# Optimization experiments

Hardware: AMD Instinct MI355X
Metric: run time of the kernel (lower is better)

Reference implementation:

```python
import jax, jax.numpy as jnp
from jax import lax
import numpy as np

NPOINT = 1024
RADIUS = 0.25
NSAMPLE = 32
USE_XYZ = True


def setup_inputs() -> dict:
    key = jax.random.key(0)
    k1, k2 = jax.random.split(key)
    xyz = jax.random.normal(k1, (8, 8192, 3), dtype=jnp.float32)
    points = jax.random.normal(k2, (8, 8192, 32), dtype=jnp.float32)
    return {"xyz": xyz, "points": points}


def furthest_point_sample(xyz, npoint):
    """Iterative FPS; returns (B, npoint, 3) sampled coordinates.
    Matches torch reference: seeded with xyz[:, 0], squared-distance metric."""
    B, N, _ = xyz.shape
    first = xyz[:, 0]  # (B, 3)
    d0 = jnp.full((B, N), 1e38, dtype=xyz.dtype)

    def step(carry, _):
        dist, last = carry  # dist: (B,N), last: (B,3)
        d2 = jnp.sum((xyz - last[:, None, :]) ** 2, axis=-1)  # (B,N)
        dist = jnp.minimum(dist, d2)
        idx = jnp.argmax(dist, axis=1)  # (B,)
        nxt = jnp.take_along_axis(xyz, idx[:, None, None], axis=1)[:, 0]  # (B,3)
        return (dist, nxt), nxt

    _, outs = lax.scan(step, (d0, first), None, length=npoint - 1)  # (npoint-1, B, 3)
    return jnp.concatenate([first[None], outs], axis=0).transpose(1, 0, 2)  # (B,npoint,3)


def ball_query(radius, nsample, xyz, new_xyz):
    """First `nsample` indices within `radius` of each center (ascending index
    order), padded with the first found index — matches pointnet2 CUDA kernel.
    Returns (B, npoint, nsample) int32."""
    N = xyz.shape[1]
    d2 = jnp.sum((new_xyz[:, :, None, :] - xyz[:, None, :, :]) ** 2, axis=-1)  # (B,npoint,N)
    mask = d2 < radius * radius
    ar = jnp.arange(N, dtype=jnp.int32)
    # top_k on negated indices -> smallest valid indices first
    score = jnp.where(mask, -ar, jnp.int32(-(N + 1)))
    vals, _ = lax.top_k(score, nsample)  # (B,npoint,nsample), descending
    valid = vals > -(N + 1)
    idx = jnp.where(valid, -vals, -vals[..., :1])  # pad with first hit
    return idx.astype(jnp.int32)


def group_points(points, idx):
    """points (B,N,C), idx (B,npoint,nsample) -> (B,npoint,nsample,C)."""
    B, npoint, nsample = idx.shape
    C = points.shape[-1]
    flat = idx.reshape(B, npoint * nsample)  # (B, npoint*nsample)
    g = jnp.take_along_axis(points, flat[:, :, None], axis=1)
    return g.reshape(B, npoint, nsample, C)


def reference(xyz, points):
    new_xyz = furthest_point_sample(xyz, NPOINT)  # (B,npoint,3)
    idx = ball_query(RADIUS, NSAMPLE, xyz, new_xyz)  # (B,npoint,nsample)
    grouped_xyz = group_points(xyz, idx) - new_xyz[:, :, None, :]  # center-relative
    grouped_points = group_points(points, idx)
    if USE_XYZ:
        new_points = jnp.concatenate([grouped_xyz, grouped_points], axis=-1)
    else:
        new_points = grouped_points
    return new_xyz, new_points
```

## Files before the change

kernel.cpp:

```cpp
#include <hip/hip_runtime.h>

#define BATCH   8
#define NPTS    8192
#define NPOINT  1024
#define NSAMPLE 32
#define CHANC   32
#define OUTC    35
#define R2      0.0625f

typedef float v2f __attribute__((ext_vector_type(2)));

template <int CTRL>
__device__ __forceinline__ float dpp_max_step(float v) {
    int r = __builtin_amdgcn_update_dpp(__float_as_int(v), __float_as_int(v),
                                        CTRL, 0xf, 0xf, false);
    return fmaxf(v, __int_as_float(r));
}
#define DPP_ROW_SHR(n)  (0x110 | (n))
#define DPP_BCAST15     0x142
#define DPP_BCAST31     0x143

__device__ __forceinline__ unsigned long long u64max(unsigned long long a,
                                                     unsigned long long b) {
    return a > b ? a : b;
}

__global__ __launch_bounds__(512) void fps_kernel(const float* __restrict__ xyz,
                                                  float* __restrict__ new_xyz) {
#pragma clang fp contract(off)
    const int b    = blockIdx.x;
    const int t    = threadIdx.x;
    const int lane = t & 63;
    const int w    = t >> 6;
    const float* bx = xyz + (size_t)b * NPTS * 3;

    __shared__ float4 pts[NPTS];
    __shared__ unsigned long long partial[2][8];

    v2f px[8], py[8], pz[8], dist[8];
    {
        float f[48];
        float4* fq = (float4*)f;
        const float4* s4 = (const float4*)bx + t * 12;
#pragma unroll
        for (int q = 0; q < 12; ++q) fq[q] = s4[q];
#pragma unroll
        for (int p = 0; p < 8; ++p) {
            px[p] = (v2f){f[6 * p + 0], f[6 * p + 3]};
            py[p] = (v2f){f[6 * p + 1], f[6 * p + 4]};
            pz[p] = (v2f){f[6 * p + 2], f[6 * p + 5]};
            dist[p] = (v2f){1e38f, 1e38f};
        }
#pragma unroll
        for (int i = 0; i < 16; ++i) {
            const int j  = t * 16 + i;
            const int js = j ^ ((j >> 4) & 7);
            pts[js] = make_float4(f[3 * i + 0], f[3 * i + 1], f[3 * i + 2], 0.0f);
        }
    }
    __syncthreads();

    float4 c0 = pts[0];
    float lx = c0.x, ly = c0.y, lz = c0.z;
    if (t == 0) {
        float* o = new_xyz + (size_t)b * NPOINT * 3;
        o[0] = lx; o[1] = ly; o[2] = lz;
    }

    for (int s = 1; s < NPOINT; ++s) {
        const v2f lx2 = (v2f){lx, lx};
        const v2f ly2 = (v2f){ly, ly};
        const v2f lz2 = (v2f){lz, lz};
        float bestv = -1.0f;
        int   bi    = 0;
#pragma unroll
        for (int p = 0; p < 8; ++p) {
            const v2f dx = px[p] - lx2;
            const v2f dy = py[p] - ly2;
            const v2f dz = pz[p] - lz2;
            const v2f d2 = (dx * dx + dy * dy) + dz * dz;
            const float d0 = fminf(dist[p].x, d2.x);
            const float d1 = fminf(dist[p].y, d2.y);
            dist[p] = (v2f){d0, d1};
            if (d0 > bestv) { bestv = d0; bi = 2 * p; }
            if (d1 > bestv) { bestv = d1; bi = 2 * p + 1; }
        }
        const int besti = (t << 4) + bi;

        float v = bestv;
        v = dpp_max_step<DPP_ROW_SHR(1)>(v);
        v = dpp_max_step<DPP_ROW_SHR(2)>(v);
        v = dpp_max_step<DPP_ROW_SHR(4)>(v);
        v = dpp_max_step<DPP_ROW_SHR(8)>(v);
        v = dpp_max_step<DPP_BCAST15>(v);
        v = dpp_max_step<DPP_BCAST31>(v);
        const float smax = __int_as_float(__builtin_amdgcn_readlane(__float_as_int(v), 63));

        const unsigned long long m = __ballot(bestv == smax);
        const int par = s & 1;
        if (lane == (int)__builtin_ctzll(m)) {
            partial[par][w] = ((unsigned long long)__float_as_uint(smax) << 32)
                              | (unsigned)(~besti);
        }
        __syncthreads();

        const unsigned long long* P = partial[par];
        const unsigned long long a0 = P[0], a1 = P[1], a2 = P[2], a3 = P[3];
        const unsigned long long a4 = P[4], a5 = P[5], a6 = P[6], a7 = P[7];
        const unsigned long long bp =
            u64max(u64max(u64max(a0, a1), u64max(a2, a3)),
                   u64max(u64max(a4, a5), u64max(a6, a7)));
        const int idx = (int)(~(unsigned)bp);
        const int js  = idx ^ ((idx >> 4) & 7);
        const float4 cw = pts[js];
        lx = cw.x; ly = cw.y; lz = cw.z;
        if (t == 0) {
            float* o = new_xyz + ((size_t)b * NPOINT + s) * 3;
            o[0] = lx; o[1] = ly; o[2] = lz;
        }
    }
}

__global__ __launch_bounds__(256) void ballgroup_kernel(const float* __restrict__ xyz,
                                                        const float* __restrict__ points,
                                                        const float* __restrict__ new_xyz,
                                                        float* __restrict__ out) {
#pragma clang fp contract(off)
    const int lane = threadIdx.x & 63;
    const int w    = threadIdx.x >> 6;
    const int gw   = blockIdx.x * 4 + w;
    const int b    = gw >> 10;

    const float* bx  = xyz + (size_t)b * NPTS * 3;
    const float* cen = new_xyz + (size_t)gw * 3;
    const float cx = cen[0], cy = cen[1], cz = cen[2];

    __shared__ int idxbuf[4][NSAMPLE];

    int k = 0;
    for (int base = 0; base < NPTS; base += 128) {
        const int j0 = base + lane;
        const int j1 = j0 + 64;
        const float a0 = bx[j0 * 3 + 0], a1 = bx[j0 * 3 + 1], a2 = bx[j0 * 3 + 2];
        const float c0 = bx[j1 * 3 + 0], c1 = bx[j1 * 3 + 1], c2 = bx[j1 * 3 + 2];
        const float dxa = a0 - cx, dya = a1 - cy, dza = a2 - cz;
        const float d2a = (dxa * dxa + dya * dya) + dza * dza;
        const float dxb = c0 - cx, dyb = c1 - cy, dzb = c2 - cz;
        const float d2b = (dxb * dxb + dyb * dyb) + dzb * dzb;
        const bool inA = d2a < R2;
        const bool inB = d2b < R2;

        const unsigned long long mA = __ballot(inA);
        int pre = __popcll(mA & ((1ull << lane) - 1ull));
        if (inA && (k + pre) < NSAMPLE) idxbuf[w][k + pre] = j0;
        k += __popcll(mA);
        if (k >= NSAMPLE) { k = NSAMPLE; break; }

        const unsigned long long mB = __ballot(inB);
        pre = __popcll(mB & ((1ull << lane) - 1ull));
        if (inB && (k + pre) < NSAMPLE) idxbuf[w][k + pre] = j1;
        k += __popcll(mB);
        if (k >= NSAMPLE) { k = NSAMPLE; break; }
    }
    const int first = idxbuf[w][0];

    float*       o    = out + (size_t)gw * NSAMPLE * OUTC;
    const float* prow = points + (size_t)b * NPTS * CHANC;
    for (int e = lane; e < NSAMPLE * OUTC; e += 64) {
        const int s = e / OUTC;
        const int c = e - s * OUTC;
        const int j = (s < k) ? idxbuf[w][s] : first;
        float v;
        if (c < 3) {
            const float cc = (c == 0) ? cx : (c == 1) ? cy : cz;
            v = bx[j * 3 + c] - cc;
        } else {
            v = prow[j * CHANC + (c - 3)];
        }
        o[e] = v;
    }
}

extern "C" void kernel_launch(void* const* d_in, const int* in_sizes, int n_in,
                              void* d_out, int out_size, void* d_ws, size_t ws_size,
                              hipStream_t stream) {
    const float* xyz    = (const float*)d_in[0];
    const float* points = (const float*)d_in[1];
    float* new_xyz    = (float*)d_out;
    float* new_points = new_xyz + (size_t)BATCH * NPOINT * 3;

    fps_kernel<<<BATCH, 512, 0, stream>>>(xyz, new_xyz);
    ballgroup_kernel<<<(BATCH * NPOINT) / 4, 256, 0, stream>>>(xyz, points, new_xyz, new_points);
}
```

Measured before the change: 1.006 ms.

## Split ball-query scan across four waves per center and merge results

Each block now handles one query center instead of four. Its four waves each scan a quarter of the 8192 points, keeping up to 32 in-radius hits per quarter, and the ordered concatenation of those lists gives the first 32 indices. The gather/output loop is then spread across all 256 threads. The aim is to shorten the serial scan per center, which stops early only after 32 hits and otherwise reads all points, at the cost of four times as many blocks, a block barrier, and waves scanning their quarters even when an earlier quarter already holds 32 hits.

```diff
diff --git a/kernel.cpp b/kernel.cpp
--- a/kernel.cpp
+++ b/kernel.cpp
@@ -126,19 +126,22 @@
                                                         const float* __restrict__ new_xyz,
                                                         float* __restrict__ out) {
 #pragma clang fp contract(off)
-    const int lane = threadIdx.x & 63;
-    const int w    = threadIdx.x >> 6;
-    const int gw   = blockIdx.x * 4 + w;
+    const int tid  = threadIdx.x;
+    const int lane = tid & 63;
+    const int r    = tid >> 6;
+    const int gw   = blockIdx.x;
     const int b    = gw >> 10;
 
     const float* bx  = xyz + (size_t)b * NPTS * 3;
     const float* cen = new_xyz + (size_t)gw * 3;
     const float cx = cen[0], cy = cen[1], cz = cen[2];
 
-    __shared__ int idxbuf[4][NSAMPLE];
+    __shared__ int qidx[4][NSAMPLE];
+    __shared__ int qcnt[4];
 
     int k = 0;
-    for (int base = 0; base < NPTS; base += 128) {
+    const int qbase = r << 11;
+    for (int base = qbase; base < qbase + 2048; base += 128) {
         const int j0 = base + lane;
         const int j1 = j0 + 64;
         const float a0 = bx[j0 * 3 + 0], a1 = bx[j0 * 3 + 1], a2 = bx[j0 * 3 + 2];
@@ -150,26 +153,43 @@
         const bool inA = d2a < R2;
         const bool inB = d2b < R2;
 
-        const unsigned long long mA = __ballot(inA);
-        int pre = __popcll(mA & ((1ull << lane) - 1ull));
-        if (inA && (k + pre) < NSAMPLE) idxbuf[w][k + pre] = j0;
-        k += __popcll(mA);
-        if (k >= NSAMPLE) { k = NSAMPLE; break; }
-
-        const unsigned long long mB = __ballot(inB);
-        pre = __popcll(mB & ((1ull << lane) - 1ull));
-        if (inB && (k + pre) < NSAMPLE) idxbuf[w][k + pre] = j1;
-        k += __popcll(mB);
-        if (k >= NSAMPLE) { k = NSAMPLE; break; }
-    }
-    const int first = idxbuf[w][0];
+        if (__any(inA || inB)) {
+            const unsigned long long mA = __ballot(inA);
+            int pre = __popcll(mA & ((1ull << lane) - 1ull));
+            if (inA && (k + pre) < NSAMPLE) qidx[r][k + pre] = j0;
+            k += __popcll(mA);
+            if (k >= NSAMPLE) { k = NSAMPLE; break; }
+
+            const unsigned long long mB = __ballot(inB);
+            pre = __popcll(mB & ((1ull << lane) - 1ull));
+            if (inB && (k + pre) < NSAMPLE) qidx[r][k + pre] = j1;
+            k += __popcll(mB);
+            if (k >= NSAMPLE) { k = NSAMPLE; break; }
+        }
+    }
+    if (lane == 0) qcnt[r] = k;
+    __syncthreads();
+
+    const int c0n = qcnt[0], c1n = qcnt[1], c2n = qcnt[2], c3n = qcnt[3];
+    const int o1 = c0n, o2 = c0n + c1n, o3 = o2 + c2n;
+    const int total = o3 + c3n;
+    const int kk = total < NSAMPLE ? total : NSAMPLE;
+    const int r0 = (c0n > 0) ? 0 : (c1n > 0) ? 1 : (c2n > 0) ? 2 : 3;
+    const int firstIdx = qidx[r0][0];
 
     float*       o    = out + (size_t)gw * NSAMPLE * OUTC;
     const float* prow = points + (size_t)b * NPTS * CHANC;
-    for (int e = lane; e < NSAMPLE * OUTC; e += 64) {
+    for (int e = tid; e < NSAMPLE * OUTC; e += 256) {
         const int s = e / OUTC;
         const int c = e - s * OUTC;
-        const int j = (s < k) ? idxbuf[w][s] : first;
+        int j;
+        if (s < kk) {
+            const int rr  = (int)(s >= o1) + (int)(s >= o2) + (int)(s >= o3);
+            const int off = (rr == 0) ? 0 : (rr == 1) ? o1 : (rr == 2) ? o2 : o3;
+            j = qidx[rr][s - off];
+        } else {
+            j = firstIdx;
+        }
         float v;
         if (c < 3) {
             const float cc = (c == 0) ? cx : (c == 1) ? cy : cz;
@@ -190,5 +210,5 @@
     float* new_points = new_xyz + (size_t)BATCH * NPOINT * 3;
 
     fps_kernel<<<BATCH, 512, 0, stream>>>(xyz, new_xyz);
-    ballgroup_kernel<<<(BATCH * NPOINT) / 4, 256, 0, stream>>>(xyz, points, new_xyz, new_points);
-}
+    ballgroup_kernel<<<BATCH * NPOINT, 256, 0, stream>>>(xyz, points, new_xyz, new_points);
+}
```

Result: no change. 1.005 ms (-0.0%).

## Stage point chunks in LDS and share them across many ball-query centers

Applied to the files above, without the earlier changes.

The ball-query kernel now handles 32 centers per block, 8 per wave. It stages 2048-point chunks of xyz into shared memory as float4 so that every point load is reused across many centers. Before, each wave scanned global xyz alone for a single center. The cost is far fewer blocks (one per 32 centers), which lowers occupancy. The scan also loses its early exit: the loop keeps visiting every chunk even after all 8 centers have filled their 32 samples, and only the per-center work is skipped.

```diff
diff --git a/kernel.cpp b/kernel.cpp
--- a/kernel.cpp
+++ b/kernel.cpp
@@ -7,6 +7,8 @@
 #define CHANC   32
 #define OUTC    35
 #define R2      0.0625f
+#define GCTR    32
+#define CHUNK   2048
 
 typedef float v2f __attribute__((ext_vector_type(2)));
 
@@ -126,58 +128,77 @@
                                                         const float* __restrict__ new_xyz,
                                                         float* __restrict__ out) {
 #pragma clang fp contract(off)
-    const int lane = threadIdx.x & 63;
-    const int w    = threadIdx.x >> 6;
-    const int gw   = blockIdx.x * 4 + w;
-    const int b    = gw >> 10;
-
-    const float* bx  = xyz + (size_t)b * NPTS * 3;
-    const float* cen = new_xyz + (size_t)gw * 3;
-    const float cx = cen[0], cy = cen[1], cz = cen[2];
-
-    __shared__ int idxbuf[4][NSAMPLE];
-
-    int k = 0;
-    for (int base = 0; base < NPTS; base += 128) {
-        const int j0 = base + lane;
-        const int j1 = j0 + 64;
-        const float a0 = bx[j0 * 3 + 0], a1 = bx[j0 * 3 + 1], a2 = bx[j0 * 3 + 2];
-        const float c0 = bx[j1 * 3 + 0], c1 = bx[j1 * 3 + 1], c2 = bx[j1 * 3 + 2];
-        const float dxa = a0 - cx, dya = a1 - cy, dza = a2 - cz;
-        const float d2a = (dxa * dxa + dya * dya) + dza * dza;
-        const float dxb = c0 - cx, dyb = c1 - cy, dzb = c2 - cz;
-        const float d2b = (dxb * dxb + dyb * dyb) + dzb * dzb;
-        const bool inA = d2a < R2;
-        const bool inB = d2b < R2;
-
-        const unsigned long long mA = __ballot(inA);
-        int pre = __popcll(mA & ((1ull << lane) - 1ull));
-        if (inA && (k + pre) < NSAMPLE) idxbuf[w][k + pre] = j0;
-        k += __popcll(mA);
-        if (k >= NSAMPLE) { k = NSAMPLE; break; }
-
-        const unsigned long long mB = __ballot(inB);
-        pre = __popcll(mB & ((1ull << lane) - 1ull));
-        if (inB && (k + pre) < NSAMPLE) idxbuf[w][k + pre] = j1;
-        k += __popcll(mB);
-        if (k >= NSAMPLE) { k = NSAMPLE; break; }
-    }
-    const int first = idxbuf[w][0];
-
-    float*       o    = out + (size_t)gw * NSAMPLE * OUTC;
+    const int tid   = threadIdx.x;
+    const int lane  = tid & 63;
+    const int w     = tid >> 6;
+    const int cbase = blockIdx.x * GCTR;
+    const int b     = cbase >> 10;
+    const float* bx = xyz + (size_t)b * NPTS * 3;
+
+    __shared__ float4 spts[CHUNK];
+    __shared__ int    qidx[GCTR][NSAMPLE];
+
+    float cxv[8], cyv[8], czv[8];
+    int   k[8];
+#pragma unroll
+    for (int c = 0; c < 8; ++c) {
+        const float* cen = new_xyz + (size_t)(cbase + w * 8 + c) * 3;
+        cxv[c] = cen[0]; cyv[c] = cen[1]; czv[c] = cen[2];
+        k[c] = 0;
+    }
+
+    for (int chunk = 0; chunk < NPTS; chunk += CHUNK) {
+        __syncthreads();
+#pragma unroll
+        for (int q = 0; q < CHUNK / 256; ++q) {
+            const int p = q * 256 + tid;
+            const int j = chunk + p;
+            spts[p] = make_float4(bx[j * 3 + 0], bx[j * 3 + 1], bx[j * 3 + 2], 0.0f);
+        }
+        __syncthreads();
+
+        for (int round = 0; round < CHUNK / 64; ++round) {
+            const float4 pt = spts[round * 64 + lane];
+            const int j = chunk + round * 64 + lane;
+#pragma unroll
+            for (int c = 0; c < 8; ++c) {
+                if (k[c] >= NSAMPLE) continue;
+                const float dx = pt.x - cxv[c];
+                const float dy = pt.y - cyv[c];
+                const float dz = pt.z - czv[c];
+                const float d2 = (dx * dx + dy * dy) + dz * dz;
+                const bool in = d2 < R2;
+                if (__any(in)) {
+                    const unsigned long long mu = __ballot(in);
+                    const int pre = __popcll(mu & ((1ull << lane) - 1ull));
+                    if (in && (k[c] + pre) < NSAMPLE)
+                        qidx[w * 8 + c][k[c] + pre] = j;
+                    k[c] += __popcll(mu);
+                }
+            }
+        }
+    }
+
     const float* prow = points + (size_t)b * NPTS * CHANC;
-    for (int e = lane; e < NSAMPLE * OUTC; e += 64) {
-        const int s = e / OUTC;
-        const int c = e - s * OUTC;
-        const int j = (s < k) ? idxbuf[w][s] : first;
-        float v;
-        if (c < 3) {
-            const float cc = (c == 0) ? cx : (c == 1) ? cy : cz;
-            v = bx[j * 3 + c] - cc;
-        } else {
-            v = prow[j * CHANC + (c - 3)];
-        }
-        o[e] = v;
+#pragma unroll
+    for (int c = 0; c < 8; ++c) {
+        const int ctr = cbase + w * 8 + c;
+        const int kk  = k[c] < NSAMPLE ? k[c] : NSAMPLE;
+        const int firstIdx = qidx[w * 8 + c][0];
+        float* o = out + (size_t)ctr * NSAMPLE * OUTC;
+        for (int e = lane; e < NSAMPLE * OUTC; e += 64) {
+            const int s  = e / OUTC;
+            const int ch = e - s * OUTC;
+            const int j  = (s < kk) ? qidx[w * 8 + c][s] : firstIdx;
+            float v;
+            if (ch < 3) {
+                const float cc = (ch == 0) ? cxv[c] : (ch == 1) ? cyv[c] : czv[c];
+                v = bx[j * 3 + ch] - cc;
+            } else {
+                v = prow[j * CHANC + (ch - 3)];
+            }
+            o[e] = v;
+        }
     }
 }
 
@@ -190,5 +211,5 @@
     float* new_points = new_xyz + (size_t)BATCH * NPOINT * 3;
 
     fps_kernel<<<BATCH, 512, 0, stream>>>(xyz, new_xyz);
-    ballgroup_kernel<<<(BATCH * NPOINT) / 4, 256, 0, stream>>>(xyz, points, new_xyz, new_points);
-}
+    ballgroup_kernel<<<(BATCH * NPOINT) / GCTR, 256, 0, stream>>>(xyz, points, new_xyz, new_points);
+}
```

Result: slower. 1.085 ms (+7.8%).

## Fuse FPS and ball-query grouping into one cooperative kernel with progress counters

Applied to the files above, without the earlier changes.

Merges the FPS and ball-query/grouping kernels into one cooperative launch. Eight blocks run FPS and publish progress through per-batch atomic counters every 8 samples. The remaining blocks cache the batch's xyz in shared memory, spin until their centroid is ready, then do the ball query and grouping. The aim is to hide the grouping work behind the serial FPS tail and to replace global xyz reads with LDS reads. The cost is a memset, a cooperative launch, fence overhead in the FPS loop, and spin-wait traffic that may contend with the FPS blocks.

```diff
diff --git a/kernel.cpp b/kernel.cpp
--- a/kernel.cpp
+++ b/kernel.cpp
@@ -7,6 +7,8 @@
 #define CHANC   32
 #define OUTC    35
 #define R2      0.0625f
+#define CPB     31
+#define NBLK    (BATCH + BATCH * CPB)
 
 typedef float v2f __attribute__((ext_vector_type(2)));
 
@@ -25,159 +27,173 @@
     return a > b ? a : b;
 }
 
-__global__ __launch_bounds__(512) void fps_kernel(const float* __restrict__ xyz,
-                                                  float* __restrict__ new_xyz) {
+__global__ __launch_bounds__(512) void fused_kernel(const float* __restrict__ xyz,
+                                                    const float* __restrict__ points,
+                                                    float* new_xyz,
+                                                    float* out,
+                                                    int* ctr) {
 #pragma clang fp contract(off)
-    const int b    = blockIdx.x;
+    __shared__ float4 pts[NPTS];
+    __shared__ unsigned long long partial[2][8];
+    __shared__ int idxbuf[8][NSAMPLE];
+
+    const int blk  = blockIdx.x;
     const int t    = threadIdx.x;
     const int lane = t & 63;
     const int w    = t >> 6;
-    const float* bx = xyz + (size_t)b * NPTS * 3;
-
-    __shared__ float4 pts[NPTS];
-    __shared__ unsigned long long partial[2][8];
-
-    v2f px[8], py[8], pz[8], dist[8];
-    {
-        float f[48];
-        float4* fq = (float4*)f;
-        const float4* s4 = (const float4*)bx + t * 12;
-#pragma unroll
-        for (int q = 0; q < 12; ++q) fq[q] = s4[q];
-#pragma unroll
-        for (int p = 0; p < 8; ++p) {
-            px[p] = (v2f){f[6 * p + 0], f[6 * p + 3]};
-            py[p] = (v2f){f[6 * p + 1], f[6 * p + 4]};
-            pz[p] = (v2f){f[6 * p + 2], f[6 * p + 5]};
-            dist[p] = (v2f){1e38f, 1e38f};
-        }
+
+    if (blk < BATCH) {
+        const int b = blk;
+        const float* bx = xyz + (size_t)b * NPTS * 3;
+
+        v2f px[8], py[8], pz[8], dist[8];
+        {
+            float f[48];
+            float4* fq = (float4*)f;
+            const float4* s4 = (const float4*)bx + t * 12;
+#pragma unroll
+            for (int q = 0; q < 12; ++q) fq[q] = s4[q];
+#pragma unroll
+            for (int p = 0; p < 8; ++p) {
+                px[p] = (v2f){f[6 * p + 0], f[6 * p + 3]};
+                py[p] = (v2f){f[6 * p + 1], f[6 * p + 4]};
+                pz[p] = (v2f){f[6 * p + 2], f[6 * p + 5]};
+                dist[p] = (v2f){1e38f, 1e38f};
+            }
+#pragma unroll
+            for (int i = 0; i < 16; ++i) {
+                const int j  = t * 16 + i;
+                const int js = j ^ ((j >> 4) & 7);
+                pts[js] = make_float4(f[3 * i + 0], f[3 * i + 1], f[3 * i + 2], 0.0f);
+            }
+        }
+        __syncthreads();
+
+        float4 c0 = pts[0];
+        float lx = c0.x, ly = c0.y, lz = c0.z;
+        if (t == 0) {
+            float* o = new_xyz + (size_t)b * NPOINT * 3;
+            o[0] = lx; o[1] = ly; o[2] = lz;
+        }
+
+        for (int s = 1; s < NPOINT; ++s) {
+            const v2f lx2 = (v2f){lx, lx};
+            const v2f ly2 = (v2f){ly, ly};
+            const v2f lz2 = (v2f){lz, lz};
+            float bestv = -1.0f;
+            int   bi    = 0;
+#pragma unroll
+            for (int p = 0; p < 8; ++p) {
+                const v2f dx = px[p] - lx2;
+                const v2f dy = py[p] - ly2;
+                const v2f dz = pz[p] - lz2;
+                const v2f d2 = (dx * dx + dy * dy) + dz * dz;
+                const float d0 = fminf(dist[p].x, d2.x);
+                const float d1 = fminf(dist[p].y, d2.y);
+                dist[p] = (v2f){d0, d1};
+                if (d0 > bestv) { bestv = d0; bi = 2 * p; }
+                if (d1 > bestv) { bestv = d1; bi = 2 * p + 1; }
+            }
+            const int besti = (t << 4) + bi;
+
+            float v = bestv;
+            v = dpp_max_step<DPP_ROW_SHR(1)>(v);
+            v = dpp_max_step<DPP_ROW_SHR(2)>(v);
+            v = dpp_max_step<DPP_ROW_SHR(4)>(v);
+            v = dpp_max_step<DPP_ROW_SHR(8)>(v);
+            v = dpp_max_step<DPP_BCAST15>(v);
+            v = dpp_max_step<DPP_BCAST31>(v);
+            const float smax = __int_as_float(__builtin_amdgcn_readlane(__float_as_int(v), 63));
+
+            const unsigned long long m = __ballot(bestv == smax);
+            const int par = s & 1;
+            if (lane == (int)__builtin_ctzll(m)) {
+                partial[par][w] = ((unsigned long long)__float_as_uint(smax) << 32)
+                                  | (unsigned)(~besti);
+            }
+            __syncthreads();
+
+            const unsigned long long* P = partial[par];
+            const unsigned long long a0 = P[0], a1 = P[1], a2 = P[2], a3 = P[3];
+            const unsigned long long a4 = P[4], a5 = P[5], a6 = P[6], a7 = P[7];
+            const unsigned long long bp =
+                u64max(u64max(u64max(a0, a1), u64max(a2, a3)),
+                       u64max(u64max(a4, a5), u64max(a6, a7)));
+            const int idx = (int)(~(unsigned)bp);
+            const int js  = idx ^ ((idx >> 4) & 7);
+            const float4 cw = pts[js];
+            lx = cw.x; ly = cw.y; lz = cw.z;
+            if (t == 0) {
+                float* o = new_xyz + ((size_t)b * NPOINT + s) * 3;
+                o[0] = lx; o[1] = ly; o[2] = lz;
+                if ((s & 7) == 7) {
+                    __threadfence();
+                    __hip_atomic_store(&ctr[b], s + 1, __ATOMIC_RELEASE,
+                                       __HIP_MEMORY_SCOPE_AGENT);
+                }
+            }
+        }
+    } else {
+        const int q  = blk - BATCH;
+        const int b  = q / CPB;
+        const int cb = q % CPB;
+        const float* bx = xyz + (size_t)b * NPTS * 3;
+
 #pragma unroll
         for (int i = 0; i < 16; ++i) {
-            const int j  = t * 16 + i;
-            const int js = j ^ ((j >> 4) & 7);
-            pts[js] = make_float4(f[3 * i + 0], f[3 * i + 1], f[3 * i + 2], 0.0f);
-        }
-    }
-    __syncthreads();
-
-    float4 c0 = pts[0];
-    float lx = c0.x, ly = c0.y, lz = c0.z;
-    if (t == 0) {
-        float* o = new_xyz + (size_t)b * NPOINT * 3;
-        o[0] = lx; o[1] = ly; o[2] = lz;
-    }
-
-    for (int s = 1; s < NPOINT; ++s) {
-        const v2f lx2 = (v2f){lx, lx};
-        const v2f ly2 = (v2f){ly, ly};
-        const v2f lz2 = (v2f){lz, lz};
-        float bestv = -1.0f;
-        int   bi    = 0;
-#pragma unroll
-        for (int p = 0; p < 8; ++p) {
-            const v2f dx = px[p] - lx2;
-            const v2f dy = py[p] - ly2;
-            const v2f dz = pz[p] - lz2;
-            const v2f d2 = (dx * dx + dy * dy) + dz * dz;
-            const float d0 = fminf(dist[p].x, d2.x);
-            const float d1 = fminf(dist[p].y, d2.y);
-            dist[p] = (v2f){d0, d1};
-            if (d0 > bestv) { bestv = d0; bi = 2 * p; }
-            if (d1 > bestv) { bestv = d1; bi = 2 * p + 1; }
-        }
-        const int besti = (t << 4) + bi;
-
-        float v = bestv;
-        v = dpp_max_step<DPP_ROW_SHR(1)>(v);
-        v = dpp_max_step<DPP_ROW_SHR(2)>(v);
-        v = dpp_max_step<DPP_ROW_SHR(4)>(v);
-        v = dpp_max_step<DPP_ROW_SHR(8)>(v);
-        v = dpp_max_step<DPP_BCAST15>(v);
-        v = dpp_max_step<DPP_BCAST31>(v);
-        const float smax = __int_as_float(__builtin_amdgcn_readlane(__float_as_int(v), 63));
-
-        const unsigned long long m = __ballot(bestv == smax);
-        const int par = s & 1;
-        if (lane == (int)__builtin_ctzll(m)) {
-            partial[par][w] = ((unsigned long long)__float_as_uint(smax) << 32)
-                              | (unsigned)(~besti);
+            const int j = i * 512 + t;
+            pts[j] = make_float4(bx[3 * j + 0], bx[3 * j + 1], bx[3 * j + 2], 0.0f);
         }
         __syncthreads();
 
-        const unsigned long long* P = partial[par];
-        const unsigned long long a0 = P[0], a1 = P[1], a2 = P[2], a3 = P[3];
-        const unsigned long long a4 = P[4], a5 = P[5], a6 = P[6], a7 = P[7];
-        const unsigned long long bp =
-            u64max(u64max(u64max(a0, a1), u64max(a2, a3)),
-                   u64max(u64max(a4, a5), u64max(a6, a7)));
-        const int idx = (int)(~(unsigned)bp);
-        const int js  = idx ^ ((idx >> 4) & 7);
-        const float4 cw = pts[js];
-        lx = cw.x; ly = cw.y; lz = cw.z;
-        if (t == 0) {
-            float* o = new_xyz + ((size_t)b * NPOINT + s) * 3;
-            o[0] = lx; o[1] = ly; o[2] = lz;
-        }
-    }
-}
-
-__global__ __launch_bounds__(256) void ballgroup_kernel(const float* __restrict__ xyz,
-                                                        const float* __restrict__ points,
-                                                        const float* __restrict__ new_xyz,
-                                                        float* __restrict__ out) {
-#pragma clang fp contract(off)
-    const int lane = threadIdx.x & 63;
-    const int w    = threadIdx.x >> 6;
-    const int gw   = blockIdx.x * 4 + w;
-    const int b    = gw >> 10;
-
-    const float* bx  = xyz + (size_t)b * NPTS * 3;
-    const float* cen = new_xyz + (size_t)gw * 3;
-    const float cx = cen[0], cy = cen[1], cz = cen[2];
-
-    __shared__ int idxbuf[4][NSAMPLE];
-
-    int k = 0;
-    for (int base = 0; base < NPTS; base += 128) {
-        const int j0 = base + lane;
-        const int j1 = j0 + 64;
-        const float a0 = bx[j0 * 3 + 0], a1 = bx[j0 * 3 + 1], a2 = bx[j0 * 3 + 2];
-        const float c0 = bx[j1 * 3 + 0], c1 = bx[j1 * 3 + 1], c2 = bx[j1 * 3 + 2];
-        const float dxa = a0 - cx, dya = a1 - cy, dza = a2 - cz;
-        const float d2a = (dxa * dxa + dya * dya) + dza * dza;
-        const float dxb = c0 - cx, dyb = c1 - cy, dzb = c2 - cz;
-        const float d2b = (dxb * dxb + dyb * dyb) + dzb * dzb;
-        const bool inA = d2a < R2;
-        const bool inB = d2b < R2;
-
-        const unsigned long long mA = __ballot(inA);
-        int pre = __popcll(mA & ((1ull << lane) - 1ull));
-        if (inA && (k + pre) < NSAMPLE) idxbuf[w][k + pre] = j0;
-        k += __popcll(mA);
-        if (k >= NSAMPLE) { k = NSAMPLE; break; }
-
-        const unsigned long long mB = __ballot(inB);
-        pre = __popcll(mB & ((1ull << lane) - 1ull));
-        if (inB && (k + pre) < NSAMPLE) idxbuf[w][k + pre] = j1;
-        k += __popcll(mB);
-        if (k >= NSAMPLE) { k = NSAMPLE; break; }
-    }
-    const int first = idxbuf[w][0];
-
-    float*       o    = out + (size_t)gw * NSAMPLE * OUTC;
-    const float* prow = points + (size_t)b * NPTS * CHANC;
-    for (int e = lane; e < NSAMPLE * OUTC; e += 64) {
-        const int s = e / OUTC;
-        const int c = e - s * OUTC;
-        const int j = (s < k) ? idxbuf[w][s] : first;
-        float v;
-        if (c < 3) {
-            const float cc = (c == 0) ? cx : (c == 1) ? cy : cz;
-            v = bx[j * 3 + c] - cc;
-        } else {
-            v = prow[j * CHANC + (c - 3)];
-        }
-        o[e] = v;
+        const float* prow = points + (size_t)b * NPTS * CHANC;
+
+        for (int s = cb * 8 + w; s < NPOINT; s += BATCH * CPB) {
+            while (__hip_atomic_load(&ctr[b], __ATOMIC_ACQUIRE,
+                                     __HIP_MEMORY_SCOPE_AGENT) <= s)
+                __builtin_amdgcn_s_sleep(8);
+
+            const int gw = b * NPOINT + s;
+            const float cx = __hip_atomic_load(&new_xyz[gw * 3 + 0],
+                                               __ATOMIC_RELAXED, __HIP_MEMORY_SCOPE_AGENT);
+            const float cy = __hip_atomic_load(&new_xyz[gw * 3 + 1],
+                                               __ATOMIC_RELAXED, __HIP_MEMORY_SCOPE_AGENT);
+            const float cz = __hip_atomic_load(&new_xyz[gw * 3 + 2],
+                                               __ATOMIC_RELAXED, __HIP_MEMORY_SCOPE_AGENT);
+
+            int k = 0;
+            for (int base = 0; base < NPTS; base += 64) {
+                const float4 p = pts[base + lane];
+                const float dx = p.x - cx;
+                const float dy = p.y - cy;
+                const float dz = p.z - cz;
+                const float d2 = (dx * dx + dy * dy) + dz * dz;
+                const bool in = d2 < R2;
+                const unsigned long long mu = __ballot(in);
+                const int pre = __popcll(mu & ((1ull << lane) - 1ull));
+                if (in && (k + pre) < NSAMPLE) idxbuf[w][k + pre] = base + lane;
+                k += __popcll(mu);
+                if (k >= NSAMPLE) { k = NSAMPLE; break; }
+            }
+            const int first = idxbuf[w][0];
+
+            float* o = out + (size_t)gw * NSAMPLE * OUTC;
+            for (int e = lane; e < NSAMPLE * OUTC; e += 64) {
+                const int sj = e / OUTC;
+                const int c  = e - sj * OUTC;
+                const int j  = (sj < k) ? idxbuf[w][sj] : first;
+                float vv;
+                if (c < 3) {
+                    const float4 pj = pts[j];
+                    const float pv = (c == 0) ? pj.x : (c == 1) ? pj.y : pj.z;
+                    const float cc = (c == 0) ? cx : (c == 1) ? cy : cz;
+                    vv = pv - cc;
+                } else {
+                    vv = prow[j * CHANC + (c - 3)];
+                }
+                o[e] = vv;
+            }
+        }
     }
 }
 
@@ -188,7 +204,12 @@
     const float* points = (const float*)d_in[1];
     float* new_xyz    = (float*)d_out;
     float* new_points = new_xyz + (size_t)BATCH * NPOINT * 3;
-
-    fps_kernel<<<BATCH, 512, 0, stream>>>(xyz, new_xyz);
-    ballgroup_kernel<<<(BATCH * NPOINT) / 4, 256, 0, stream>>>(xyz, points, new_xyz, new_points);
-}
+    int*   ctr        = (int*)d_ws;
+
+    hipMemsetAsync(ctr, 0, BATCH * sizeof(int), stream);
+
+    void* args[] = {(void*)&xyz, (void*)&points, (void*)&new_xyz,
+                    (void*)&new_points, (void*)&ctr};
+    hipLaunchCooperativeKernel((const void*)fused_kernel, dim3(NBLK), dim3(512),
+                               args, 0, stream);
+}
```

New measurement: 1.191 ms. 1.18x slower.
